# Kernel tuning notes

Measured on AMD Instinct MI355X. Metric: run time of the kernel, lower is better.

The kernel has to match this reference:

```python
import jax, jax.numpy as jnp
import numpy as np

M = 8
EPS = 1e-5


def _bn(x, gamma, beta):
    # x: [T, N, C]; torch BatchNorm1d on [T, C, N] (training mode) normalizes
    # over batch and length dims -> axes (0, 1) here, biased variance.
    mean = jnp.mean(x, axis=(0, 1))
    var = jnp.var(x, axis=(0, 1))
    return (x - mean) * jax.lax.rsqrt(var + EPS) * gamma + beta


def setup_inputs() -> dict:
    key = jax.random.key(0)
    T, N, E = 128, 256, 128
    ks = jax.random.split(key, 16)
    s = 1.0 / np.sqrt(E)
    inp = {
        "node": jax.random.normal(ks[0], (T, N, E), dtype=jnp.float32),
        "Wq": jax.random.uniform(ks[1], (E, E), jnp.float32, -s, s),
        "bq": jax.random.uniform(ks[2], (E,), jnp.float32, -s, s),
        "Wk": jax.random.uniform(ks[3], (E, E), jnp.float32, -s, s),
        "bk": jax.random.uniform(ks[4], (E,), jnp.float32, -s, s),
        "Wv": jax.random.uniform(ks[5], (E, E), jnp.float32, -s, s),
        "bv": jax.random.uniform(ks[6], (E,), jnp.float32, -s, s),
        "Ww": jax.random.uniform(ks[7], (E, E), jnp.float32, -s, s),
        "bw": jax.random.uniform(ks[8], (E,), jnp.float32, -s, s),
        "Wf1": jax.random.uniform(ks[9], (4 * E, E), jnp.float32, -s, s),
        "bf1": jax.random.uniform(ks[10], (4 * E,), jnp.float32, -s, s),
        "Wf2": jax.random.uniform(ks[11], (E, 4 * E), jnp.float32, -0.5 * s, 0.5 * s),
        "bf2": jax.random.uniform(ks[12], (E,), jnp.float32, -0.5 * s, 0.5 * s),
        "g1": jnp.ones((E,), jnp.float32),
        "be1": jnp.zeros((E,), jnp.float32),
        "g2": jnp.ones((E,), jnp.float32),
        "be2": jnp.zeros((E,), jnp.float32),
        "temp_len": T,
    }
    return inp


def reference(node, Wq, bq, Wk, bk, Wv, bv, Ww, bw, Wf1, bf1, Wf2, bf2,
              g1, be1, g2, be2, temp_len):
    T, N, E = node.shape
    D = E // M          # head dim = 16
    dk = E / M          # softmax scale denominator (embedding_size / M)

    q = (node @ Wq.T + bq).reshape(T, N, M, D)
    k = (node @ Wk.T + bk).reshape(T, N, M, D)
    v = (node @ Wv.T + bv).reshape(T, N, M, D)

    # scores[t,n,j,m] = sum_d q[t,n,m,d]*k[t,j,m,d] / sqrt(dk)
    scores = jnp.einsum('tnmd,tjmd->tnjm', q, k) / jnp.sqrt(jnp.float32(dk))
    attn = jax.nn.softmax(scores, axis=2)  # softmax over key dim (dim=2)

    # out[t,n,m,d] = sum_j attn[t,n,j,m] * v[t,j,m,d]
    out = jnp.einsum('tnjm,tjmd->tnmd', attn, v).reshape(T, N, E)

    x = out @ Ww.T + bw + node
    x = _bn(x, g1, be1)

    x1 = jax.nn.relu(x @ Wf1.T + bf1) @ Wf2.T + bf2
    x = x + x1
    x = _bn(x, g2, be2)
    return x
```

## Files before the change

### kernel.cpp

```cpp
#include <hip/hip_runtime.h>
#include <stdint.h>

typedef unsigned int  uint32;
typedef unsigned short u16;
typedef __attribute__((ext_vector_type(8))) short short8;
typedef __attribute__((ext_vector_type(4))) float f32x4;
typedef __attribute__((ext_vector_type(4))) _Float16 half4;

__device__ __forceinline__ float bits2f(uint32 u){ union{uint32 u; float f;} c; c.u=u; return c.f; }
__device__ __forceinline__ uint32 f2bits(float f){ union{uint32 u; float f;} c; c.f=f; return c.u; }
__device__ __forceinline__ u16 f2b(float f){ uint32 u=f2bits(f); return (u16)((u + 0x7FFFu + ((u>>16)&1u))>>16); }
__device__ __forceinline__ float b2f(u16 h){ return bits2f(((uint32)h)<<16); }
__device__ __forceinline__ u16 f2h(float f){ _Float16 h=(_Float16)f; union{u16 u; _Float16 h;} c; c.h=h; return c.u; }
__device__ __forceinline__ float4 ld4f(const float* p){ return *(const float4*)p; }
#define BLO(u) bits2f((u)<<16)
#define BHI(u) bits2f((u)&0xFFFF0000u)

#define QKS 24

__device__ __forceinline__ void load_ab(const float* __restrict__ gacc,
                                        const float* __restrict__ gam,
                                        const float* __restrict__ bet,
                                        float* sA, float* sB, int t)
{
  if (t < 128) {
    const float mean = gacc[t] * (1.f/32768.f);
    const float var  = gacc[128 + t] * (1.f/32768.f) - mean * mean;
    const float rstd = rsqrtf(var + 1e-5f);
    const float Ac = gam[t] * rstd;
    sA[t] = Ac;
    sB[t] = bet[t] - mean * Ac;
  }
  __syncthreads();
}

template<int OMODE, int RES, bool RELU, bool AF32, bool WF32, bool BNA, bool STATS, int JT>
__device__ __forceinline__ void gemm_tile(
    u16* As, u16* Ws, const float* sA, const float* sB, float* pS, float* pQ,
    const void* Ain, const void* W, const float* bias, const void* res,
    float* gacc_out, void* out, int row0, int col0, int K, int Nout,
    float oscale, int t)
{
  constexpr int WROWS = JT * 32;
  const int L = t & 63, w = t >> 6;
  const int wrow = (w >> 1) * 64, wcol = (w & 1) * (JT * 16);
  const int lm = L & 15, lg = L >> 4;

  f32x4 acc[4][JT];
#pragma unroll
  for (int i = 0; i < 4; ++i)
#pragma unroll
    for (int j = 0; j < JT; ++j) acc[i][j] = (f32x4){0.f,0.f,0.f,0.f};

  const int srow = t >> 1, skc = (t & 1) * 32;
  const u16*   Ab = (const u16*)Ain + (size_t)(row0 + srow) * K + skc;
  const float* Af = (const float*)Ain + (size_t)(row0 + srow) * K + skc;
  u16* Asp = As + srow * 72 + skc;
  constexpr int TPR = 256 / WROWS;
  const int wsrow = t / TPR, wskc = (t % TPR) * (64 / TPR);
  const u16*   Wp  = (const u16*)W + (size_t)(col0 + wsrow) * K + wskc;
  const float* Wpf = (const float*)W + (size_t)(col0 + wsrow) * K + wskc;
  u16* Wsp = Ws + wsrow * 72 + wskc;
  constexpr int NW = (64 / TPR) / 8;

  short8 ga[4]; short8 gw[NW];
  float4 fa[4][2]; float4 fw[NW][2];

  auto load_chunk = [&](int k0) {
    if constexpr (AF32) {
#pragma unroll
      for (int i = 0; i < 4; ++i) {
        fa[i][0] = ld4f(Af + k0 + i*8);
        fa[i][1] = ld4f(Af + k0 + i*8 + 4);
      }
    } else {
#pragma unroll
      for (int i = 0; i < 4; ++i) ga[i] = *(const short8*)(Ab + k0 + i*8);
    }
    if constexpr (WF32) {
#pragma unroll
      for (int i = 0; i < NW; ++i) {
        fw[i][0] = ld4f(Wpf + k0 + i*8);
        fw[i][1] = ld4f(Wpf + k0 + i*8 + 4);
      }
    } else {
#pragma unroll
      for (int i = 0; i < NW; ++i) gw[i] = *(const short8*)(Wp + k0 + i*8);
    }
  };

  auto write_chunk = [&](int k0) {
    if constexpr (AF32) {
#pragma unroll
      for (int i = 0; i < 4; ++i) {
        short8 s;
        s[0]=(short)f2b(fa[i][0].x); s[1]=(short)f2b(fa[i][0].y);
        s[2]=(short)f2b(fa[i][0].z); s[3]=(short)f2b(fa[i][0].w);
        s[4]=(short)f2b(fa[i][1].x); s[5]=(short)f2b(fa[i][1].y);
        s[6]=(short)f2b(fa[i][1].z); s[7]=(short)f2b(fa[i][1].w);
        *(short8*)(Asp + i*8) = s;
      }
    } else if constexpr (BNA) {
#pragma unroll
      for (int i = 0; i < 4; ++i) {
        const int c = skc + k0 + i*8;
        const short8 x8 = ga[i];
        const float4 A0 = *(const float4*)&sA[c], A1 = *(const float4*)&sA[c+4];
        const float4 B0 = *(const float4*)&sB[c], B1 = *(const float4*)&sB[c+4];
        short8 s;
        s[0]=(short)f2b(b2f((u16)x8[0])*A0.x+B0.x); s[1]=(short)f2b(b2f((u16)x8[1])*A0.y+B0.y);
        s[2]=(short)f2b(b2f((u16)x8[2])*A0.z+B0.z); s[3]=(short)f2b(b2f((u16)x8[3])*A0.w+B0.w);
        s[4]=(short)f2b(b2f((u16)x8[4])*A1.x+B1.x); s[5]=(short)f2b(b2f((u16)x8[5])*A1.y+B1.y);
        s[6]=(short)f2b(b2f((u16)x8[6])*A1.z+B1.z); s[7]=(short)f2b(b2f((u16)x8[7])*A1.w+B1.w);
        *(short8*)(Asp + i*8) = s;
      }
    } else {
#pragma unroll
      for (int i = 0; i < 4; ++i) *(short8*)(Asp + i*8) = ga[i];
    }
    if constexpr (WF32) {
#pragma unroll
      for (int i = 0; i < NW; ++i) {
        short8 s;
        s[0]=(short)f2b(fw[i][0].x); s[1]=(short)f2b(fw[i][0].y);
        s[2]=(short)f2b(fw[i][0].z); s[3]=(short)f2b(fw[i][0].w);
        s[4]=(short)f2b(fw[i][1].x); s[5]=(short)f2b(fw[i][1].y);
        s[6]=(short)f2b(fw[i][1].z); s[7]=(short)f2b(fw[i][1].w);
        *(short8*)(Wsp + i*8) = s;
      }
    } else {
#pragma unroll
      for (int i = 0; i < NW; ++i) *(short8*)(Wsp + i*8) = gw[i];
    }
  };

  load_chunk(0);
  for (int k0 = 0; k0 < K; k0 += 64) {
    __syncthreads();
    write_chunk(k0);
    __syncthreads();
    if (k0 + 64 < K) load_chunk(k0 + 64);
#pragma unroll
    for (int ks = 0; ks < 64; ks += 32) {
      short8 af[4], wf[JT];
#pragma unroll
      for (int i = 0; i < 4; ++i)
        af[i] = *(const short8*)(As + (wrow + i*16 + lm) * 72 + ks + lg*8);
#pragma unroll
      for (int j = 0; j < JT; ++j)
        wf[j] = *(const short8*)(Ws + (wcol + j*16 + lm) * 72 + ks + lg*8);
#pragma unroll
      for (int i = 0; i < 4; ++i)
#pragma unroll
        for (int j = 0; j < JT; ++j)
          acc[i][j] = __builtin_amdgcn_mfma_f32_16x16x32_bf16(af[i], wf[j], acc[i][j], 0, 0, 0);
    }
  }

  float bj[JT];
#pragma unroll
  for (int j = 0; j < JT; ++j) bj[j] = bias[col0 + wcol + j*16 + lm];

  float stS[JT], stQ[JT];
#pragma unroll
  for (int j = 0; j < JT; ++j) { stS[j] = 0.f; stQ[j] = 0.f; }

#pragma unroll
  for (int i = 0; i < 4; ++i) {
    const int rowb = row0 + wrow + i*16 + lg*4;
#pragma unroll
    for (int j = 0; j < JT; ++j) {
      const int col = col0 + wcol + j*16 + lm;
      float ra = 0.f, rb = 0.f;
      if constexpr (RES == 3) { ra = sA[col & 127]; rb = sB[col & 127]; }
      if constexpr (OMODE == 3) {
        const int tt = rowb >> 8, n0 = rowb & 255;
        const int mh = col >> 4, d = col & 15;
        uint2 o;
        o.x = (uint32)f2h(acc[i][j][0] + bj[j]) | ((uint32)f2h(acc[i][j][1] + bj[j]) << 16);
        o.y = (uint32)f2h(acc[i][j][2] + bj[j]) | ((uint32)f2h(acc[i][j][3] + bj[j]) << 16);
        *(uint2*)((u16*)out + (((size_t)tt*8 + mh)*16 + d)*256 + n0) = o;
      } else {
#pragma unroll
        for (int r = 0; r < 4; ++r) {
          const int row = rowb + r;
          float v = acc[i][j][r] + bj[j];
          if constexpr (RES == 1) v += ((const float*)res)[(size_t)row*128 + col];
          if constexpr (RES == 3) v += b2f(((const u16*)res)[(size_t)row*128 + col]) * ra + rb;
          if constexpr (RELU) v = fmaxf(v, 0.f);
          if constexpr (STATS) { stS[j] += v; stQ[j] += v*v; }
          if constexpr (OMODE == 2) {
            const int tt = row >> 8, n = row & 255, mh = col >> 4, d = col & 15;
            ((u16*)out)[(((size_t)tt*8 + mh)*256 + n)*16 + d] = f2h(v * oscale);
          } else {
            ((u16*)out)[(size_t)row * Nout + col] = f2b(v);
          }
        }
      }
    }
  }

  if constexpr (STATS) {
    __syncthreads();
    if (t < 128) { pS[t] = 0.f; pQ[t] = 0.f; }
    __syncthreads();
#pragma unroll
    for (int j = 0; j < JT; ++j) {
      const int col = col0 + wcol + j*16 + lm;
      atomicAdd(&pS[col], stS[j]);
      atomicAdd(&pQ[col], stQ[j]);
    }
    __syncthreads();
    if (t < 128) {
      atomicAdd(&gacc_out[t],       pS[t]);
      atomicAdd(&gacc_out[128 + t], pQ[t]);
    }
  }
}

__global__ __launch_bounds__(256)
void qkv_k(const float* __restrict__ node,
           const float* __restrict__ Wq, const float* __restrict__ bq,
           const float* __restrict__ Wk, const float* __restrict__ bk,
           const float* __restrict__ Wv, const float* __restrict__ bv,
           const float* __restrict__ Ww, const float* __restrict__ Wf1,
           const float* __restrict__ Wf2,
           u16* __restrict__ qb, u16* __restrict__ kb, u16* __restrict__ vb,
           u16* __restrict__ wb, float* __restrict__ accbuf)
{
  const int bid = blockIdx.x, t = threadIdx.x;
  if (bid < 256) {
    __shared__ u16 As[2*128*72];
    __shared__ u16 Ws[2*128*72];
    const int row0 = bid * 128;
    const int L = t & 63, w = t >> 6;
    const int wrow = (w >> 1) * 64, wcol = (w & 1) * 64;
    const int lm = L & 15, lg = L >> 4;
    const int srow = t >> 1, skc = (t & 1) * 32;

    {
      const float* Af = node + (size_t)(row0 + srow) * 128 + skc;
#pragma unroll
      for (int c = 0; c < 2; ++c) {
        u16* Asp = As + c*128*72 + srow*72 + skc;
#pragma unroll
        for (int i = 0; i < 4; ++i) {
          const float4 fa = ld4f(Af + c*64 + i*8);
          const float4 fb = ld4f(Af + c*64 + i*8 + 4);
          short8 s;
          s[0]=(short)f2b(fa.x); s[1]=(short)f2b(fa.y); s[2]=(short)f2b(fa.z); s[3]=(short)f2b(fa.w);
          s[4]=(short)f2b(fb.x); s[5]=(short)f2b(fb.y); s[6]=(short)f2b(fb.z); s[7]=(short)f2b(fb.w);
          *(short8*)(Asp + i*8) = s;
        }
      }
    }

    const float* WY0 = Wq; const float* WY1 = Wk; const float* WY2 = Wv;
    float4 fw[4][2];
    {
      const float* Wp = WY0 + (size_t)srow*128 + skc;
#pragma unroll
      for (int i = 0; i < 4; ++i) { fw[i][0] = ld4f(Wp + i*8); fw[i][1] = ld4f(Wp + i*8 + 4); }
    }

    f32x4 acc[4][4];
#pragma unroll
    for (int i = 0; i < 4; ++i)
#pragma unroll
      for (int j = 0; j < 4; ++j) acc[i][j] = (f32x4){0.f,0.f,0.f,0.f};

    for (int g = 0; g < 6; ++g) {
      u16* Wsp = Ws + (g&1)*128*72 + srow*72 + skc;
#pragma unroll
      for (int i = 0; i < 4; ++i) {
        short8 s;
        s[0]=(short)f2b(fw[i][0].x); s[1]=(short)f2b(fw[i][0].y);
        s[2]=(short)f2b(fw[i][0].z); s[3]=(short)f2b(fw[i][0].w);
        s[4]=(short)f2b(fw[i][1].x); s[5]=(short)f2b(fw[i][1].y);
        s[6]=(short)f2b(fw[i][1].z); s[7]=(short)f2b(fw[i][1].w);
        *(short8*)(Wsp + i*8) = s;
      }
      __syncthreads();
      if (g < 5) {
        const int gn = g + 1;
        const float* WYn = (gn < 2) ? WY0 : (gn < 4) ? WY1 : WY2;
        const float* Wp = WYn + (size_t)srow*128 + (gn & 1)*64 + skc;
#pragma unroll
        for (int i = 0; i < 4; ++i) { fw[i][0] = ld4f(Wp + i*8); fw[i][1] = ld4f(Wp + i*8 + 4); }
      }
      const u16* Ab = As + (g&1)*128*72;
      const u16* Wb = Ws + (g&1)*128*72;
#pragma unroll
      for (int ks = 0; ks < 64; ks += 32) {
        short8 af[4], wf[4];
#pragma unroll
        for (int i = 0; i < 4; ++i)
          af[i] = *(const short8*)(Ab + (wrow + i*16 + lm) * 72 + ks + lg*8);
#pragma unroll
        for (int j = 0; j < 4; ++j)
          wf[j] = *(const short8*)(Wb + (wcol + j*16 + lm) * 72 + ks + lg*8);
#pragma unroll
        for (int i = 0; i < 4; ++i)
#pragma unroll
          for (int j = 0; j < 4; ++j)
            acc[i][j] = __builtin_amdgcn_mfma_f32_16x16x32_bf16(af[i], wf[j], acc[i][j], 0, 0, 0);
      }
      if (g & 1) {
        const int y = g >> 1;
        const float* bias = (y == 0) ? bq : (y == 1) ? bk : bv;
        u16* outp = (y == 0) ? qb : (y == 1) ? kb : vb;
        const float osc = (y == 0) ? 0.36067376022224085f : 1.f;
        float bj[4];
#pragma unroll
        for (int j = 0; j < 4; ++j) bj[j] = bias[wcol + j*16 + lm];
        if (y < 2) {
#pragma unroll
          for (int i = 0; i < 4; ++i) {
            const int rowb = row0 + wrow + i*16 + lg*4;
#pragma unroll
            for (int j = 0; j < 4; ++j) {
              const int col = wcol + j*16 + lm;
              const int mh = col >> 4, d = col & 15;
#pragma unroll
              for (int r = 0; r < 4; ++r) {
                const int row = rowb + r;
                const int tt2 = row >> 8, n = row & 255;
                outp[(((size_t)tt2*8 + mh)*256 + n)*16 + d] = f2h((acc[i][j][r] + bj[j]) * osc);
              }
            }
          }
        } else {
#pragma unroll
          for (int i = 0; i < 4; ++i) {
            const int rowb = row0 + wrow + i*16 + lg*4;
            const int tt2 = rowb >> 8, n0 = rowb & 255;
#pragma unroll
            for (int j = 0; j < 4; ++j) {
              const int col = wcol + j*16 + lm;
              const int mh = col >> 4, d = col & 15;
              uint2 o;
              o.x = (uint32)f2h(acc[i][j][0] + bj[j]) | ((uint32)f2h(acc[i][j][1] + bj[j]) << 16);
              o.y = (uint32)f2h(acc[i][j][2] + bj[j]) | ((uint32)f2h(acc[i][j][3] + bj[j]) << 16);
              *(uint2*)(outp + (((size_t)tt2*8 + mh)*16 + d)*256 + n0) = o;
            }
          }
        }
#pragma unroll
        for (int i = 0; i < 4; ++i)
#pragma unroll
          for (int j = 0; j < 4; ++j) acc[i][j] = (f32x4){0.f,0.f,0.f,0.f};
      }
    }
  } else if (bid < 400) {
    const int i = (bid - 256) * 256 + t;
    const float4* src; u16* dst;
    if      (i <  4096) { src = (const float4*)Ww  + i;         dst = wb +  49152 + (size_t)i*4; }
    else if (i < 20480) { src = (const float4*)Wf1 + (i-4096);  dst = wb +  65536 + (size_t)(i-4096)*4; }
    else                { src = (const float4*)Wf2 + (i-20480); dst = wb + 131072 + (size_t)(i-20480)*4; }
    float4 v = *src;
    uint2 o;
    o.x = (uint32)f2b(v.x) | ((uint32)f2b(v.y) << 16);
    o.y = (uint32)f2b(v.z) | ((uint32)f2b(v.w) << 16);
    *(uint2*)dst = o;
  } else {
    accbuf[t] = 0.f;
    accbuf[256 + t] = 0.f;
  }
}

__global__ __launch_bounds__(256)
void oproj_k(const u16* __restrict__ ab, const u16* __restrict__ wwb,
             const float* __restrict__ bw, const float* __restrict__ node,
             float* __restrict__ accbuf, u16* __restrict__ xb)
{
  __shared__ u16 As[128*72];
  __shared__ u16 Ws[64*72];
  __shared__ __align__(16) float sA[128], sB[128];
  __shared__ float pS[128], pQ[128];
  gemm_tile<0,1,false,false,false,false,true,2>(As,Ws,sA,sB,pS,pQ, ab, wwb, bw,
      node, accbuf, xb, blockIdx.x*128, blockIdx.y*64, 128, 128, 1.f, threadIdx.x);
}

#define HS2_LD 264
#define AS_LD 136
#define WS_LD 72

__global__ __launch_bounds__(512, 4)
void ffn_k(const u16* __restrict__ xb, const u16* __restrict__ wf1b,
           const float* __restrict__ bf1, const u16* __restrict__ wf2b,
           const float* __restrict__ bf2, const float* __restrict__ accbuf,
           const float* __restrict__ g1, const float* __restrict__ be1,
           float* __restrict__ acc2, u16* __restrict__ x2b)
{
  __shared__ u16 Hs[64*HS2_LD];
  __shared__ u16 As[64*AS_LD];
  __shared__ u16 Ws[128*WS_LD];
  __shared__ __align__(16) float sA[128], sB[128];
  __shared__ float pS[128], pQ[128];

  const int t = threadIdx.x;
  const int row0 = blockIdx.x * 64;
  load_ab(accbuf, g1, be1, sA, sB, t);

  {
    const int r = t >> 3, seg = (t & 7) * 16;
    const u16* src = xb + (size_t)(row0 + r) * 128 + seg;
    u16* dst = As + r * AS_LD + seg;
#pragma unroll
    for (int h = 0; h < 2; ++h) {
      const short8 x8 = *(const short8*)(src + h*8);
      const int c = seg + h*8;
      const float4 A0 = *(const float4*)&sA[c], A1 = *(const float4*)&sA[c+4];
      const float4 B0 = *(const float4*)&sB[c], B1 = *(const float4*)&sB[c+4];
      short8 s;
      s[0]=(short)f2b(b2f((u16)x8[0])*A0.x+B0.x); s[1]=(short)f2b(b2f((u16)x8[1])*A0.y+B0.y);
      s[2]=(short)f2b(b2f((u16)x8[2])*A0.z+B0.z); s[3]=(short)f2b(b2f((u16)x8[3])*A0.w+B0.w);
      s[4]=(short)f2b(b2f((u16)x8[4])*A1.x+B1.x); s[5]=(short)f2b(b2f((u16)x8[5])*A1.y+B1.y);
      s[6]=(short)f2b(b2f((u16)x8[6])*A1.z+B1.z); s[7]=(short)f2b(b2f((u16)x8[7])*A1.w+B1.w);
      *(short8*)(dst + h*8) = s;
    }
  }

  const int w = t >> 6, L = t & 63, lm = L & 15, lg = L >> 4;
  const int wcol = w * 16;
  const int wr = t >> 2, kc = (t & 3) * 16;

  auto wsrc = [&](int g) -> const u16* {
    const int half = g >> 3, cc = g & 7;
    if (cc < 4) return wf1b + (size_t)((2*half + (cc>>1))*128 + wr)*128 + (cc&1)*64 + kc;
    return wf2b + (size_t)wr*512 + half*256 + (cc-4)*64 + kc;
  };

  f32x4 accF[4];
  f32x4 acc2r[4];
#pragma unroll
  for (int i = 0; i < 4; ++i) {
    accF[i]  = (f32x4){0.f,0.f,0.f,0.f};
    acc2r[i] = (f32x4){0.f,0.f,0.f,0.f};
  }

  short8 gw0 = *(const short8*)(wsrc(0));
  short8 gw1 = *(const short8*)(wsrc(0) + 8);

  for (int g = 0; g < 16; ++g) {
    const int cc = g & 7;
    const bool is1 = (cc < 4);
    __syncthreads();
    *(short8*)(Ws + wr*WS_LD + kc)     = gw0;
    *(short8*)(Ws + wr*WS_LD + kc + 8) = gw1;
    __syncthreads();
    if (g < 15) {
      gw0 = *(const short8*)(wsrc(g+1));
      gw1 = *(const short8*)(wsrc(g+1) + 8);
    }
    const u16* Abase = is1 ? (As + ((size_t)(cc & 1) * 64))
                           : (Hs + ((size_t)(cc - 4) * 64));
    const int ald = is1 ? AS_LD : HS2_LD;
#pragma unroll
    for (int ks = 0; ks < 64; ks += 32) {
      short8 af[4], wf;
#pragma unroll
      for (int i = 0; i < 4; ++i)
        af[i] = *(const short8*)(Abase + (i*16 + lm) * ald + ks + lg*8);
      wf = *(const short8*)(Ws + (wcol + lm) * WS_LD + ks + lg*8);
      if (is1) {
#pragma unroll
        for (int i = 0; i < 4; ++i)
          accF[i] = __builtin_amdgcn_mfma_f32_16x16x32_bf16(af[i], wf, accF[i], 0, 0, 0);
      } else {
#pragma unroll
        for (int i = 0; i < 4; ++i)
          acc2r[i] = __builtin_amdgcn_mfma_f32_16x16x32_bf16(af[i], wf, acc2r[i], 0, 0, 0);
      }
    }
    if (is1 && (cc & 1)) {
      const int half = g >> 3;
      const int ct = 2*half + (cc >> 1);
      const int lct = cc >> 1;
      const float b1 = bf1[ct*128 + wcol + lm];
#pragma unroll
      for (int i = 0; i < 4; ++i) {
#pragma unroll
        for (int r = 0; r < 4; ++r) {
          const int row = i*16 + lg*4 + r;
          Hs[row*HS2_LD + lct*128 + wcol + lm] = f2b(fmaxf(accF[i][r] + b1, 0.f));
        }
        accF[i] = (f32x4){0.f,0.f,0.f,0.f};
      }
    }
  }

  const int col = wcol + lm;
  const float b2 = bf2[col];
  const float ra = sA[col], rb = sB[col];
  float stS = 0.f, stQ = 0.f;
#pragma unroll
  for (int i = 0; i < 4; ++i) {
#pragma unroll
    for (int r = 0; r < 4; ++r) {
      const int row = row0 + i*16 + lg*4 + r;
      float v = acc2r[i][r] + b2 + b2f(xb[(size_t)row*128 + col]) * ra + rb;
      stS += v; stQ += v*v;
      x2b[(size_t)row*128 + col] = f2b(v);
    }
  }
  __syncthreads();
  if (t < 128) { pS[t] = 0.f; pQ[t] = 0.f; }
  __syncthreads();
  atomicAdd(&pS[col], stS);
  atomicAdd(&pQ[col], stQ);
  __syncthreads();
  if (t < 128) {
    atomicAdd(&acc2[t],       pS[t]);
    atomicAdd(&acc2[128 + t], pQ[t]);
  }
}

__global__ __launch_bounds__(256)
void attn_k(const u16* __restrict__ q, const u16* __restrict__ k,
            const u16* __restrict__ v, u16* __restrict__ ab)
{
  __shared__ __align__(16) u16 Qs[256*QKS];
  __shared__ __align__(16) u16 Ks[256*QKS];
  __shared__ __align__(16) u16 Vt[16*264];
  const int tm = blockIdx.x, tt = tm >> 3, m = tm & 7;
  const int t = threadIdx.x;

  const uint4* qg = (const uint4*)(q + (size_t)tm*4096);
  const uint4* kg = (const uint4*)(k + (size_t)tm*4096);
  const uint4* vg = (const uint4*)(v + (size_t)tm*4096);
#pragma unroll
  for (int p = t; p < 512; p += 256) {
    const uint4 a = qg[p], b = kg[p], c = vg[p];
    const int row = p >> 1, h = (p & 1) * 8;
    *(uint4*)(Qs + row*QKS + h) = a;
    *(uint4*)(Ks + row*QKS + h) = b;
    *(uint4*)(Vt + (p >> 5)*264 + (p & 31)*8) = c;
  }
  __syncthreads();

  const int w = t >> 6, L = t & 63, lm = L & 15, quad = L >> 4;

  half4 vf[16];
#pragma unroll
  for (int jt = 0; jt < 16; ++jt)
    vf[jt] = *(const half4*)(Vt + lm*264 + jt*16 + quad*4);

  for (int nt = 0; nt < 4; ++nt) {
    const half4 bq = *(const half4*)(Qs + ((w*4 + nt)*16 + lm)*QKS + quad*4);
    f32x4 s[16];
#pragma unroll
    for (int jt = 0; jt < 16; ++jt) {
      const half4 af = *(const half4*)(Ks + (jt*16 + lm)*QKS + quad*4);
      s[jt] = __builtin_amdgcn_mfma_f32_16x16x16f16(af, bq, (f32x4){0.f,0.f,0.f,0.f}, 0, 0, 0);
    }
    float mx = s[0][0];
#pragma unroll
    for (int jt = 0; jt < 16; ++jt)
#pragma unroll
      for (int r = 0; r < 4; ++r) mx = fmaxf(mx, s[jt][r]);
    mx = fmaxf(mx, __shfl_xor(mx, 16));
    mx = fmaxf(mx, __shfl_xor(mx, 32));
    float ls = 0.f;
#pragma unroll
    for (int jt = 0; jt < 16; ++jt)
#pragma unroll
      for (int r = 0; r < 4; ++r) { const float p = exp2f(s[jt][r] - mx); s[jt][r] = p; ls += p; }
    ls += __shfl_xor(ls, 16);
    ls += __shfl_xor(ls, 32);

    f32x4 oacc = {0.f,0.f,0.f,0.f};
#pragma unroll
    for (int jt = 0; jt < 16; ++jt) {
      half4 pf;
      pf[0] = (_Float16)s[jt][0]; pf[1] = (_Float16)s[jt][1];
      pf[2] = (_Float16)s[jt][2]; pf[3] = (_Float16)s[jt][3];
      oacc = __builtin_amdgcn_mfma_f32_16x16x16f16(pf, vf[jt], oacc, 0, 0, 0);
    }
    const int q0 = w*64 + nt*16 + quad*4;
#pragma unroll
    for (int r = 0; r < 4; ++r) {
      const float lr = __shfl(ls, quad*4 + r);
      ab[((size_t)tt*256 + q0 + r)*128 + m*16 + lm] = f2b(oacc[r] / lr);
    }
  }
}

__global__ __launch_bounds__(256)
void bn_final(const uint2* __restrict__ x2, const float* __restrict__ gacc,
              const float* __restrict__ gam, const float* __restrict__ bet,
              float* __restrict__ out)
{
  __shared__ __align__(16) float sA[128], sB[128];
  const int t = threadIdx.x;
  load_ab(gacc, gam, bet, sA, sB, t);
#pragma unroll 2
  for (int kk = 0; kk < 8; ++kk) {
    const size_t idx = (size_t)blockIdx.x * 2048 + kk * 256 + t;
    const uint2 u = x2[idx];
    const int c = (int)((idx & 31) * 4);
    const f32x4 A = *(const f32x4*)&sA[c];
    const f32x4 B = *(const f32x4*)&sB[c];
    f32x4 o;
    o[0] = BLO(u.x)*A[0] + B[0];
    o[1] = BHI(u.x)*A[1] + B[1];
    o[2] = BLO(u.y)*A[2] + B[2];
    o[3] = BHI(u.y)*A[3] + B[3];
    *(f32x4*)(out + idx*4) = o;
  }
}

extern "C" void kernel_launch(void* const* d_in, const int* in_sizes, int n_in,
                              void* d_out, int out_size, void* d_ws, size_t ws_size,
                              hipStream_t stream)
{
  (void)in_sizes; (void)n_in; (void)out_size; (void)ws_size;
  const float* node = (const float*)d_in[0];
  const float* Wq  = (const float*)d_in[1];  const float* bq  = (const float*)d_in[2];
  const float* Wk  = (const float*)d_in[3];  const float* bk  = (const float*)d_in[4];
  const float* Wv  = (const float*)d_in[5];  const float* bv  = (const float*)d_in[6];
  const float* Ww  = (const float*)d_in[7];  const float* bw  = (const float*)d_in[8];
  const float* Wf1 = (const float*)d_in[9];  const float* bf1 = (const float*)d_in[10];
  const float* Wf2 = (const float*)d_in[11]; const float* bf2 = (const float*)d_in[12];
  const float* g1  = (const float*)d_in[13]; const float* be1 = (const float*)d_in[14];
  const float* g2  = (const float*)d_in[15]; const float* be2 = (const float*)d_in[16];
  float* out = (float*)d_out;
  char* ws = (char*)d_ws;

  u16* wb  = (u16*)(ws + 0);
  u16* qb  = (u16*)(ws + 524288);
  u16* kb  = (u16*)(ws + 8912896);
  u16* vb  = (u16*)(ws + 17301504);
  u16* ab  = (u16*)(ws + 25690112);
  u16* xb  = (u16*)(ws + 34078720);
  u16* x2b = (u16*)(ws + 42467328);
  float* accbuf = (float*)(ws + 50855936);

  u16* wwb = wb + 49152;  u16* wf1b = wb + 65536; u16* wf2b = wb + 131072;

  dim3 blk(256);

  qkv_k<<<dim3(401), blk, 0, stream>>>(node, Wq,bq, Wk,bk, Wv,bv, Ww, Wf1, Wf2,
                                       qb, kb, vb, wb, accbuf);
  attn_k<<<dim3(1024), blk, 0, stream>>>(qb, kb, vb, ab);
  oproj_k<<<dim3(256,2), blk, 0, stream>>>(ab, wwb, bw, node, accbuf, xb);
  ffn_k<<<dim3(512), dim3(512), 0, stream>>>(xb, wf1b, bf1, wf2b, bf2,
                                             accbuf, g1, be1, accbuf + 256, x2b);
  bn_final<<<dim3(512), blk, 0, stream>>>((const uint2*)x2b, accbuf + 256, g2, be2, out);
}
```

Baseline: 200.4 us.

## Halve QKV row tile and rewrite output projection as single-shot 512-thread kernel

Result: no change. 202.0 us (+0.8%).

```diff
diff --git a/kernel.cpp b/kernel.cpp
--- a/kernel.cpp
+++ b/kernel.cpp
@@ -32,190 +32,6 @@
     sB[t] = bet[t] - mean * Ac;
   }
   __syncthreads();
-}
-
-template<int OMODE, int RES, bool RELU, bool AF32, bool WF32, bool BNA, bool STATS, int JT>
-__device__ __forceinline__ void gemm_tile(
-    u16* As, u16* Ws, const float* sA, const float* sB, float* pS, float* pQ,
-    const void* Ain, const void* W, const float* bias, const void* res,
-    float* gacc_out, void* out, int row0, int col0, int K, int Nout,
-    float oscale, int t)
-{
-  constexpr int WROWS = JT * 32;
-  const int L = t & 63, w = t >> 6;
-  const int wrow = (w >> 1) * 64, wcol = (w & 1) * (JT * 16);
-  const int lm = L & 15, lg = L >> 4;
-
-  f32x4 acc[4][JT];
-#pragma unroll
-  for (int i = 0; i < 4; ++i)
-#pragma unroll
-    for (int j = 0; j < JT; ++j) acc[i][j] = (f32x4){0.f,0.f,0.f,0.f};
-
-  const int srow = t >> 1, skc = (t & 1) * 32;
-  const u16*   Ab = (const u16*)Ain + (size_t)(row0 + srow) * K + skc;
-  const float* Af = (const float*)Ain + (size_t)(row0 + srow) * K + skc;
-  u16* Asp = As + srow * 72 + skc;
-  constexpr int TPR = 256 / WROWS;
-  const int wsrow = t / TPR, wskc = (t % TPR) * (64 / TPR);
-  const u16*   Wp  = (const u16*)W + (size_t)(col0 + wsrow) * K + wskc;
-  const float* Wpf = (const float*)W + (size_t)(col0 + wsrow) * K + wskc;
-  u16* Wsp = Ws + wsrow * 72 + wskc;
-  constexpr int NW = (64 / TPR) / 8;
-
-  short8 ga[4]; short8 gw[NW];
-  float4 fa[4][2]; float4 fw[NW][2];
-
-  auto load_chunk = [&](int k0) {
-    if constexpr (AF32) {
-#pragma unroll
-      for (int i = 0; i < 4; ++i) {
-        fa[i][0] = ld4f(Af + k0 + i*8);
-        fa[i][1] = ld4f(Af + k0 + i*8 + 4);
-      }
-    } else {
-#pragma unroll
-      for (int i = 0; i < 4; ++i) ga[i] = *(const short8*)(Ab + k0 + i*8);
-    }
-    if constexpr (WF32) {
-#pragma unroll
-      for (int i = 0; i < NW; ++i) {
-        fw[i][0] = ld4f(Wpf + k0 + i*8);
-        fw[i][1] = ld4f(Wpf + k0 + i*8 + 4);
-      }
-    } else {
-#pragma unroll
-      for (int i = 0; i < NW; ++i) gw[i] = *(const short8*)(Wp + k0 + i*8);
-    }
-  };
-
-  auto write_chunk = [&](int k0) {
-    if constexpr (AF32) {
-#pragma unroll
-      for (int i = 0; i < 4; ++i) {
-        short8 s;
-        s[0]=(short)f2b(fa[i][0].x); s[1]=(short)f2b(fa[i][0].y);
-        s[2]=(short)f2b(fa[i][0].z); s[3]=(short)f2b(fa[i][0].w);
-        s[4]=(short)f2b(fa[i][1].x); s[5]=(short)f2b(fa[i][1].y);
-        s[6]=(short)f2b(fa[i][1].z); s[7]=(short)f2b(fa[i][1].w);
-        *(short8*)(Asp + i*8) = s;
-      }
-    } else if constexpr (BNA) {
-#pragma unroll
-      for (int i = 0; i < 4; ++i) {
-        const int c = skc + k0 + i*8;
-        const short8 x8 = ga[i];
-        const float4 A0 = *(const float4*)&sA[c], A1 = *(const float4*)&sA[c+4];
-        const float4 B0 = *(const float4*)&sB[c], B1 = *(const float4*)&sB[c+4];
-        short8 s;
-        s[0]=(short)f2b(b2f((u16)x8[0])*A0.x+B0.x); s[1]=(short)f2b(b2f((u16)x8[1])*A0.y+B0.y);
-        s[2]=(short)f2b(b2f((u16)x8[2])*A0.z+B0.z); s[3]=(short)f2b(b2f((u16)x8[3])*A0.w+B0.w);
-        s[4]=(short)f2b(b2f((u16)x8[4])*A1.x+B1.x); s[5]=(short)f2b(b2f((u16)x8[5])*A1.y+B1.y);
-        s[6]=(short)f2b(b2f((u16)x8[6])*A1.z+B1.z); s[7]=(short)f2b(b2f((u16)x8[7])*A1.w+B1.w);
-        *(short8*)(Asp + i*8) = s;
-      }
-    } else {
-#pragma unroll
-      for (int i = 0; i < 4; ++i) *(short8*)(Asp + i*8) = ga[i];
-    }
-    if constexpr (WF32) {
-#pragma unroll
-      for (int i = 0; i < NW; ++i) {
-        short8 s;
-        s[0]=(short)f2b(fw[i][0].x); s[1]=(short)f2b(fw[i][0].y);
-        s[2]=(short)f2b(fw[i][0].z); s[3]=(short)f2b(fw[i][0].w);
-        s[4]=(short)f2b(fw[i][1].x); s[5]=(short)f2b(fw[i][1].y);
-        s[6]=(short)f2b(fw[i][1].z); s[7]=(short)f2b(fw[i][1].w);
-        *(short8*)(Wsp + i*8) = s;
-      }
-    } else {
-#pragma unroll
-      for (int i = 0; i < NW; ++i) *(short8*)(Wsp + i*8) = gw[i];
-    }
-  };
-
-  load_chunk(0);
-  for (int k0 = 0; k0 < K; k0 += 64) {
-    __syncthreads();
-    write_chunk(k0);
-    __syncthreads();
-    if (k0 + 64 < K) load_chunk(k0 + 64);
-#pragma unroll
-    for (int ks = 0; ks < 64; ks += 32) {
-      short8 af[4], wf[JT];
-#pragma unroll
-      for (int i = 0; i < 4; ++i)
-        af[i] = *(const short8*)(As + (wrow + i*16 + lm) * 72 + ks + lg*8);
-#pragma unroll
-      for (int j = 0; j < JT; ++j)
-        wf[j] = *(const short8*)(Ws + (wcol + j*16 + lm) * 72 + ks + lg*8);
-#pragma unroll
-      for (int i = 0; i < 4; ++i)
-#pragma unroll
-        for (int j = 0; j < JT; ++j)
-          acc[i][j] = __builtin_amdgcn_mfma_f32_16x16x32_bf16(af[i], wf[j], acc[i][j], 0, 0, 0);
-    }
-  }
-
-  float bj[JT];
-#pragma unroll
-  for (int j = 0; j < JT; ++j) bj[j] = bias[col0 + wcol + j*16 + lm];
-
-  float stS[JT], stQ[JT];
-#pragma unroll
-  for (int j = 0; j < JT; ++j) { stS[j] = 0.f; stQ[j] = 0.f; }
-
-#pragma unroll
-  for (int i = 0; i < 4; ++i) {
-    const int rowb = row0 + wrow + i*16 + lg*4;
-#pragma unroll
-    for (int j = 0; j < JT; ++j) {
-      const int col = col0 + wcol + j*16 + lm;
-      float ra = 0.f, rb = 0.f;
-      if constexpr (RES == 3) { ra = sA[col & 127]; rb = sB[col & 127]; }
-      if constexpr (OMODE == 3) {
-        const int tt = rowb >> 8, n0 = rowb & 255;
-        const int mh = col >> 4, d = col & 15;
-        uint2 o;
-        o.x = (uint32)f2h(acc[i][j][0] + bj[j]) | ((uint32)f2h(acc[i][j][1] + bj[j]) << 16);
-        o.y = (uint32)f2h(acc[i][j][2] + bj[j]) | ((uint32)f2h(acc[i][j][3] + bj[j]) << 16);
-        *(uint2*)((u16*)out + (((size_t)tt*8 + mh)*16 + d)*256 + n0) = o;
-      } else {
-#pragma unroll
-        for (int r = 0; r < 4; ++r) {
-          const int row = rowb + r;
-          float v = acc[i][j][r] + bj[j];
-          if constexpr (RES == 1) v += ((const float*)res)[(size_t)row*128 + col];
-          if constexpr (RES == 3) v += b2f(((const u16*)res)[(size_t)row*128 + col]) * ra + rb;
-          if constexpr (RELU) v = fmaxf(v, 0.f);
-          if constexpr (STATS) { stS[j] += v; stQ[j] += v*v; }
-          if constexpr (OMODE == 2) {
-            const int tt = row >> 8, n = row & 255, mh = col >> 4, d = col & 15;
-            ((u16*)out)[(((size_t)tt*8 + mh)*256 + n)*16 + d] = f2h(v * oscale);
-          } else {
-            ((u16*)out)[(size_t)row * Nout + col] = f2b(v);
-          }
-        }
-      }
-    }
-  }
-
-  if constexpr (STATS) {
-    __syncthreads();
-    if (t < 128) { pS[t] = 0.f; pQ[t] = 0.f; }
-    __syncthreads();
-#pragma unroll
-    for (int j = 0; j < JT; ++j) {
-      const int col = col0 + wcol + j*16 + lm;
-      atomicAdd(&pS[col], stS[j]);
-      atomicAdd(&pQ[col], stQ[j]);
-    }
-    __syncthreads();
-    if (t < 128) {
-      atomicAdd(&gacc_out[t],       pS[t]);
-      atomicAdd(&gacc_out[128 + t], pQ[t]);
-    }
-  }
 }
 
 __global__ __launch_bounds__(256)
@@ -229,22 +45,23 @@
            u16* __restrict__ wb, float* __restrict__ accbuf)
 {
   const int bid = blockIdx.x, t = threadIdx.x;
-  if (bid < 256) {
-    __shared__ u16 As[2*128*72];
+  if (bid < 512) {
+    __shared__ u16 As[2*64*72];
     __shared__ u16 Ws[2*128*72];
-    const int row0 = bid * 128;
+    const int row0 = bid * 64;
     const int L = t & 63, w = t >> 6;
-    const int wrow = (w >> 1) * 64, wcol = (w & 1) * 64;
+    const int wrow = (w & 1) * 32, wcol = (w >> 1) * 64;
     const int lm = L & 15, lg = L >> 4;
+    const int arow = t >> 2, akc = (t & 3) * 16;
     const int srow = t >> 1, skc = (t & 1) * 32;
 
     {
-      const float* Af = node + (size_t)(row0 + srow) * 128 + skc;
+      const float* Af = node + (size_t)(row0 + arow) * 128 + akc;
 #pragma unroll
       for (int c = 0; c < 2; ++c) {
-        u16* Asp = As + c*128*72 + srow*72 + skc;
-#pragma unroll
-        for (int i = 0; i < 4; ++i) {
+        u16* Asp = As + c*64*72 + arow*72 + akc;
+#pragma unroll
+        for (int i = 0; i < 2; ++i) {
           const float4 fa = ld4f(Af + c*64 + i*8);
           const float4 fb = ld4f(Af + c*64 + i*8 + 4);
           short8 s;
@@ -263,9 +80,9 @@
       for (int i = 0; i < 4; ++i) { fw[i][0] = ld4f(Wp + i*8); fw[i][1] = ld4f(Wp + i*8 + 4); }
     }
 
-    f32x4 acc[4][4];
-#pragma unroll
-    for (int i = 0; i < 4; ++i)
+    f32x4 acc[2][4];
+#pragma unroll
+    for (int i = 0; i < 2; ++i)
 #pragma unroll
       for (int j = 0; j < 4; ++j) acc[i][j] = (f32x4){0.f,0.f,0.f,0.f};
 
@@ -288,19 +105,19 @@
 #pragma unroll
         for (int i = 0; i < 4; ++i) { fw[i][0] = ld4f(Wp + i*8); fw[i][1] = ld4f(Wp + i*8 + 4); }
       }
-      const u16* Ab = As + (g&1)*128*72;
+      const u16* Ab = As + (g&1)*64*72;
       const u16* Wb = Ws + (g&1)*128*72;
 #pragma unroll
       for (int ks = 0; ks < 64; ks += 32) {
-        short8 af[4], wf[4];
-#pragma unroll
-        for (int i = 0; i < 4; ++i)
+        short8 af[2], wf[4];
+#pragma unroll
+        for (int i = 0; i < 2; ++i)
           af[i] = *(const short8*)(Ab + (wrow + i*16 + lm) * 72 + ks + lg*8);
 #pragma unroll
         for (int j = 0; j < 4; ++j)
           wf[j] = *(const short8*)(Wb + (wcol + j*16 + lm) * 72 + ks + lg*8);
 #pragma unroll
-        for (int i = 0; i < 4; ++i)
+        for (int i = 0; i < 2; ++i)
 #pragma unroll
           for (int j = 0; j < 4; ++j)
             acc[i][j] = __builtin_amdgcn_mfma_f32_16x16x32_bf16(af[i], wf[j], acc[i][j], 0, 0, 0);
@@ -315,7 +132,7 @@
         for (int j = 0; j < 4; ++j) bj[j] = bias[wcol + j*16 + lm];
         if (y < 2) {
 #pragma unroll
-          for (int i = 0; i < 4; ++i) {
+          for (int i = 0; i < 2; ++i) {
             const int rowb = row0 + wrow + i*16 + lg*4;
 #pragma unroll
             for (int j = 0; j < 4; ++j) {
@@ -331,7 +148,7 @@
           }
         } else {
 #pragma unroll
-          for (int i = 0; i < 4; ++i) {
+          for (int i = 0; i < 2; ++i) {
             const int rowb = row0 + wrow + i*16 + lg*4;
             const int tt2 = rowb >> 8, n0 = rowb & 255;
 #pragma unroll
@@ -346,13 +163,13 @@
           }
         }
 #pragma unroll
-        for (int i = 0; i < 4; ++i)
+        for (int i = 0; i < 2; ++i)
 #pragma unroll
           for (int j = 0; j < 4; ++j) acc[i][j] = (f32x4){0.f,0.f,0.f,0.f};
       }
     }
-  } else if (bid < 400) {
-    const int i = (bid - 256) * 256 + t;
+  } else if (bid < 656) {
+    const int i = (bid - 512) * 256 + t;
     const float4* src; u16* dst;
     if      (i <  4096) { src = (const float4*)Ww  + i;         dst = wb +  49152 + (size_t)i*4; }
     else if (i < 20480) { src = (const float4*)Wf1 + (i-4096);  dst = wb +  65536 + (size_t)(i-4096)*4; }
@@ -368,17 +185,75 @@
   }
 }
 
-__global__ __launch_bounds__(256)
+__global__ __launch_bounds__(512, 4)
 void oproj_k(const u16* __restrict__ ab, const u16* __restrict__ wwb,
              const float* __restrict__ bw, const float* __restrict__ node,
              float* __restrict__ accbuf, u16* __restrict__ xb)
 {
-  __shared__ u16 As[128*72];
-  __shared__ u16 Ws[64*72];
-  __shared__ __align__(16) float sA[128], sB[128];
+  __shared__ __align__(16) u16 As2[128*136];
+  __shared__ __align__(16) u16 Ws2[64*136];
   __shared__ float pS[128], pQ[128];
-  gemm_tile<0,1,false,false,false,false,true,2>(As,Ws,sA,sB,pS,pQ, ab, wwb, bw,
-      node, accbuf, xb, blockIdx.x*128, blockIdx.y*64, 128, 128, 1.f, threadIdx.x);
+  const int t = threadIdx.x, bid = blockIdx.x;
+  const int w = t >> 6, L = t & 63, lm = L & 15, lg = L >> 4;
+  const int row0 = (bid >> 1) * 128, col0 = (bid & 1) * 64;
+
+  {
+    const int r = t >> 2, seg = (t & 3) * 32;
+    const u16* src = ab + (size_t)(row0 + r) * 128 + seg;
+    u16* dst = As2 + r * 136 + seg;
+#pragma unroll
+    for (int h = 0; h < 4; ++h)
+      *(short8*)(dst + h*8) = *(const short8*)(src + h*8);
+  }
+  {
+    const int r = t >> 3, seg = (t & 7) * 16;
+    const u16* src = wwb + (size_t)(col0 + r) * 128 + seg;
+    u16* dst = Ws2 + r * 136 + seg;
+#pragma unroll
+    for (int h = 0; h < 2; ++h)
+      *(short8*)(dst + h*8) = *(const short8*)(src + h*8);
+  }
+  __syncthreads();
+
+  const int wrow = (w >> 2) * 64, wcol = (w & 3) * 16;
+  f32x4 acc[4];
+#pragma unroll
+  for (int i = 0; i < 4; ++i) acc[i] = (f32x4){0.f,0.f,0.f,0.f};
+#pragma unroll
+  for (int ks = 0; ks < 128; ks += 32) {
+    short8 af[4], wf;
+#pragma unroll
+    for (int i = 0; i < 4; ++i)
+      af[i] = *(const short8*)(As2 + (wrow + i*16 + lm)*136 + ks + lg*8);
+    wf = *(const short8*)(Ws2 + (wcol + lm)*136 + ks + lg*8);
+#pragma unroll
+    for (int i = 0; i < 4; ++i)
+      acc[i] = __builtin_amdgcn_mfma_f32_16x16x32_bf16(af[i], wf, acc[i], 0, 0, 0);
+  }
+
+  const int col = col0 + wcol + lm;
+  const float bj = bw[col];
+  float stS = 0.f, stQ = 0.f;
+#pragma unroll
+  for (int i = 0; i < 4; ++i) {
+#pragma unroll
+    for (int r = 0; r < 4; ++r) {
+      const int row = row0 + wrow + i*16 + lg*4 + r;
+      float v = acc[i][r] + bj + node[(size_t)row*128 + col];
+      stS += v; stQ += v*v;
+      xb[(size_t)row*128 + col] = f2b(v);
+    }
+  }
+  __syncthreads();
+  if (t < 128) { pS[t] = 0.f; pQ[t] = 0.f; }
+  __syncthreads();
+  atomicAdd(&pS[col], stS);
+  atomicAdd(&pQ[col], stQ);
+  __syncthreads();
+  if (t < 128) {
+    atomicAdd(&accbuf[t],       pS[t]);
+    atomicAdd(&accbuf[128 + t], pQ[t]);
+  }
 }
 
 #define HS2_LD 264
@@ -640,10 +515,10 @@
 
   dim3 blk(256);
 
-  qkv_k<<<dim3(401), blk, 0, stream>>>(node, Wq,bq, Wk,bk, Wv,bv, Ww, Wf1, Wf2,
+  qkv_k<<<dim3(657), blk, 0, stream>>>(node, Wq,bq, Wk,bk, Wv,bv, Ww, Wf1, Wf2,
                                        qb, kb, vb, wb, accbuf);
   attn_k<<<dim3(1024), blk, 0, stream>>>(qb, kb, vb, ab);
-  oproj_k<<<dim3(256,2), blk, 0, stream>>>(ab, wwb, bw, node, accbuf, xb);
+  oproj_k<<<dim3(512), dim3(512), 0, stream>>>(ab, wwb, bw, node, accbuf, xb);
   ffn_k<<<dim3(512), dim3(512), 0, stream>>>(xb, wf1b, bf1, wf2b, bf2,
                                              accbuf, g1, be1, accbuf + 256, x2b);
   bn_final<<<dim3(512), blk, 0, stream>>>((const uint2*)x2b, accbuf + 256, g2, be2, out);
```
